# Optimization experiments

Hardware: AMD Instinct MI355X
Metric: run time of the kernel (lower is better)

Reference implementation:

```python
import jax, jax.numpy as jnp
import numpy as np

B, D, H = 4096, 2048, 2048

def setup_inputs() -> dict:
    key = jax.random.key(0)
    ks = jax.random.split(key, 16)
    s = 0.02  # small scale to keep tanh/sigmoid out of saturation
    inp = {
        'input_': jax.random.normal(ks[0], (B, D), jnp.float32),
        'h_prev': jax.random.normal(ks[1], (B, H), jnp.float32),
        'c_prev': jax.random.normal(ks[2], (B, H), jnp.float32),
        'w_xi': jax.random.normal(ks[3], (D, H), jnp.float32) * s,
        'w_hi': jax.random.normal(ks[4], (H, H), jnp.float32) * s,
        'w_ci': jax.random.normal(ks[5], (H, H), jnp.float32) * s,
        'w_xf': jax.random.normal(ks[6], (D, H), jnp.float32) * s,
        'w_hf': jax.random.normal(ks[7], (H, H), jnp.float32) * s,
        'w_cf': jax.random.normal(ks[8], (H, H), jnp.float32) * s,
        'w_xg': jax.random.normal(ks[9], (D, H), jnp.float32) * s,
        'w_hg': jax.random.normal(ks[10], (H, H), jnp.float32) * s,
        'w_xo': jax.random.normal(ks[11], (D, H), jnp.float32) * s,
        'w_ho': jax.random.normal(ks[12], (H, H), jnp.float32) * s,
        'w_co': jax.random.normal(ks[13], (H, H), jnp.float32) * s,
        'w_c':  jax.random.normal(ks[14], (H, H), jnp.float32) * s,
        'w_i':  jax.random.normal(ks[15], (D, H), jnp.float32) * s,
        'b_i': jnp.zeros((H,), jnp.float32),
        'b_f': jnp.zeros((H,), jnp.float32),
        'b_g': jnp.zeros((H,), jnp.float32),
        'b_o': jnp.zeros((H,), jnp.float32),
    }
    return inp

def reference(input_, h_prev, c_prev,
              w_xi, w_hi, w_ci, w_xf, w_hf, w_cf, w_xg, w_hg,
              w_xo, w_ho, w_co, w_c, w_i,
              b_i, b_f, b_g, b_o):
    # Fuse the x- and h-path GEMMs into concatenated matmuls (math-identical).
    wx = jnp.concatenate([w_xi, w_xf, w_xg, w_xo, w_i], axis=1)   # [D, 5H]
    wh = jnp.concatenate([w_hi, w_hf, w_hg, w_ho], axis=1)        # [H, 4H]
    wc = jnp.concatenate([w_ci, w_cf], axis=1)                    # [H, 2H]
    xz = input_ @ wx                                              # [B, 5H]
    hz = h_prev @ wh                                              # [B, 4H]
    cz = c_prev @ wc                                              # [B, 2H]
    Hd = w_hi.shape[0]
    i = xz[:, 0*Hd:1*Hd] + hz[:, 0*Hd:1*Hd] + cz[:, 0*Hd:1*Hd] + b_i
    f = xz[:, 1*Hd:2*Hd] + hz[:, 1*Hd:2*Hd] + cz[:, 1*Hd:2*Hd] + b_f
    g = xz[:, 2*Hd:3*Hd] + hz[:, 2*Hd:3*Hd] + b_g
    c = jax.nn.sigmoid(f) * c_prev + jax.nn.sigmoid(i) * jnp.tanh(g)
    o = xz[:, 3*Hd:4*Hd] + hz[:, 3*Hd:4*Hd] + c @ w_co + b_o
    h = jnp.tanh(o) * (jnp.tanh(c) @ w_c + xz[:, 4*Hd:5*Hd])
    return (h, c)
```

## Files before the change

### kernel.cpp

```cpp
#include <hip/hip_runtime.h>
#include <cstdint>
#include <cstddef>

typedef unsigned short u16;
typedef __bf16 bf16x8 __attribute__((ext_vector_type(8)));
typedef float f32x4 __attribute__((ext_vector_type(4)));
typedef u16 u16x8 __attribute__((ext_vector_type(8)));

#define B_DIM 4096
#define H_DIM 2048
#define BH 8388608

__device__ __forceinline__ float b2f(u16 x) {
  union { uint32_t u; float f; } v;
  v.u = ((uint32_t)x) << 16;
  return v.f;
}
__device__ __forceinline__ u16 f2b(float f) {
  union { float f; uint32_t u; } v;
  v.f = f;
  uint32_t r = v.u + 0x7FFFu + ((v.u >> 16) & 1u);
  return (u16)(r >> 16);
}
__device__ __forceinline__ float sigm(float x) { return 1.0f / (1.0f + __expf(-x)); }

typedef __attribute__((address_space(1))) void gv_t;
typedef __attribute__((address_space(3))) void lv_t;
__device__ __forceinline__ void g2lds16(const void* g, void* l) {
  __builtin_amdgcn_global_load_lds((gv_t*)g, (lv_t*)l, 16, 0, 0);
}

struct CvtParams { const float* src[3]; u16* dst[3]; };

__global__ __launch_bounds__(256) void cvt_k(CvtParams p) {
  const float* __restrict__ s = p.src[blockIdx.y];
  u16* __restrict__ d = p.dst[blockIdx.y];
  size_t idx = ((size_t)blockIdx.x * 256 + threadIdx.x) * 8;
  float4 a = *(const float4*)(s + idx);
  float4 b = *(const float4*)(s + idx + 4);
  u16x8 o;
  o[0] = f2b(a.x); o[1] = f2b(a.y); o[2] = f2b(a.z); o[3] = f2b(a.w);
  o[4] = f2b(b.x); o[5] = f2b(b.y); o[6] = f2b(b.z); o[7] = f2b(b.w);
  *(u16x8*)(d + idx) = o;
}

struct TransParams {
  const float* src[13];
  u16* dst[13];
  int dstride[13];
};

__global__ __launch_bounds__(256) void transpose_k(TransParams p) {
  __shared__ u16 lds[64][72];
  const int mat = blockIdx.z;
  const float* __restrict__ src = p.src[mat];
  u16* __restrict__ dst = p.dst[mat];
  const int dstride = p.dstride[mat];
  const int tk = blockIdx.y * 64;
  const int tn = blockIdx.x * 64;
  const int t = threadIdx.x;
  const int lr = t >> 3;
  const int lc = (t & 7) * 8;
#pragma unroll
  for (int half = 0; half < 2; half++) {
    int r = lr + half * 32;
    const float4* g = (const float4*)(src + (size_t)(tk + r) * 2048 + tn + lc);
    float4 a = g[0], b = g[1];
    u16x8 t8;
    t8[0] = f2b(a.x); t8[1] = f2b(a.y); t8[2] = f2b(a.z); t8[3] = f2b(a.w);
    t8[4] = f2b(b.x); t8[5] = f2b(b.y); t8[6] = f2b(b.z); t8[7] = f2b(b.w);
    *(u16x8*)&lds[r][lc] = t8;
  }
  __syncthreads();
#pragma unroll
  for (int half = 0; half < 2; half++) {
    int n = lr + half * 32;
    u16x8 tmp;
#pragma unroll
    for (int j = 0; j < 8; j++) tmp[j] = lds[lc + j][n];
    *(u16x8*)(dst + (size_t)(tn + n) * dstride + tk + lc) = tmp;
  }
}

struct GemmDesc {
  const u16* A0; const u16* A1; const u16* A2;
  const u16* Wt; u16* C; int nseg; int addin;
};
struct GemmParams { GemmDesc d[5]; };

__global__ __launch_bounds__(256) void gemm_multi(GemmParams p) {
  const GemmDesc d = p.d[blockIdx.z];
  const int nseg = d.nseg;
  const long Ktot = (long)nseg * 2048;

  __shared__ u16 ldsA[128 * 32];
  __shared__ u16 ldsB[128 * 32];

  const int t = threadIdx.x;
  const int wave = t >> 6, lane = t & 63;
  const int m0 = blockIdx.y * 128, n0 = blockIdx.x * 128;

  const int sr = lane >> 2;
  const int sc = (lane & 3) * 8;
  u16* lA0 = &ldsA[wave * 1024];
  u16* lA1 = lA0 + 512;
  u16* lB0 = &ldsB[wave * 1024];
  u16* lB1 = lB0 + 512;
  const size_t rA0 = (size_t)(m0 + wave * 32 + sr);
  const size_t rB0 = (size_t)(n0 + wave * 32 + sr);

  const int fm = lane & 15, fk = (lane >> 4) * 8;
  const int wm = (wave >> 1) * 64, wn = (wave & 1) * 64;

  f32x4 acc[4][4];
#pragma unroll
  for (int i = 0; i < 4; i++)
#pragma unroll
    for (int j = 0; j < 4; j++) acc[i][j] = (f32x4)0.0f;

  for (int seg = 0; seg < nseg; ++seg) {
    const u16* As = (seg == 0) ? d.A0 : ((seg == 1) ? d.A1 : d.A2);
    const u16* pA0 = As + rA0 * 2048 + sc;
    const u16* pA1 = pA0 + 16 * 2048;
    const u16* pB0 = d.Wt + rB0 * Ktot + (size_t)seg * 2048 + sc;
    const u16* pB1 = pB0 + 16 * Ktot;
    for (int kk = 0; kk < 2048; kk += 32) {
      __syncthreads();
      g2lds16(pA0, lA0);
      g2lds16(pA1, lA1);
      g2lds16(pB0, lB0);
      g2lds16(pB1, lB1);
      __syncthreads();
      bf16x8 af[4], bfr[4];
#pragma unroll
      for (int i = 0; i < 4; i++)
        af[i] = *(const bf16x8*)&ldsA[(wm + i * 16 + fm) * 32 + fk];
#pragma unroll
      for (int j = 0; j < 4; j++)
        bfr[j] = *(const bf16x8*)&ldsB[(wn + j * 16 + fm) * 32 + fk];
#pragma unroll
      for (int i = 0; i < 4; i++)
#pragma unroll
        for (int j = 0; j < 4; j++)
          acc[i][j] = __builtin_amdgcn_mfma_f32_16x16x32_bf16(af[i], bfr[j], acc[i][j], 0, 0, 0);
      pA0 += 32; pA1 += 32; pB0 += 32; pB1 += 32;
    }
  }

  const int quad = lane >> 4;
#pragma unroll
  for (int i = 0; i < 4; i++) {
#pragma unroll
    for (int j = 0; j < 4; j++) {
#pragma unroll
      for (int r = 0; r < 4; r++) {
        size_t row = (size_t)(m0 + wm + i * 16 + quad * 4 + r);
        size_t col = (size_t)(n0 + wn + j * 16 + fm);
        size_t cidx = row * 2048 + col;
        float v = acc[i][j][r];
        if (d.addin) v += b2f(d.C[cidx]);
        d.C[cidx] = f2b(v);
      }
    }
  }
}

__global__ __launch_bounds__(256) void ew1_k(
    u16* __restrict__ zi, const u16* __restrict__ zf, u16* __restrict__ zg,
    const float* __restrict__ cprev, const float* __restrict__ bi,
    const float* __restrict__ bff, const float* __restrict__ bg,
    float* __restrict__ c_out) {
  size_t idx = ((size_t)blockIdx.x * 256 + threadIdx.x) * 8;
  int col = (int)(idx & (H_DIM - 1));
  u16x8 vzi = *(const u16x8*)(zi + idx);
  u16x8 vzf = *(const u16x8*)(zf + idx);
  u16x8 vzg = *(const u16x8*)(zg + idx);
  float4 cp0 = *(const float4*)(cprev + idx);
  float4 cp1 = *(const float4*)(cprev + idx + 4);
  float4 bi0 = *(const float4*)(bi + col), bi1 = *(const float4*)(bi + col + 4);
  float4 bf0 = *(const float4*)(bff + col), bf1 = *(const float4*)(bff + col + 4);
  float4 bg0 = *(const float4*)(bg + col), bg1 = *(const float4*)(bg + col + 4);
  float cpv[8] = {cp0.x, cp0.y, cp0.z, cp0.w, cp1.x, cp1.y, cp1.z, cp1.w};
  float biv[8] = {bi0.x, bi0.y, bi0.z, bi0.w, bi1.x, bi1.y, bi1.z, bi1.w};
  float bfv[8] = {bf0.x, bf0.y, bf0.z, bf0.w, bf1.x, bf1.y, bf1.z, bf1.w};
  float bgv[8] = {bg0.x, bg0.y, bg0.z, bg0.w, bg1.x, bg1.y, bg1.z, bg1.w};
  float cv[8], tcv[8];
#pragma unroll
  for (int e = 0; e < 8; e++) {
    float iv = b2f(vzi[e]) + biv[e];
    float fv = b2f(vzf[e]) + bfv[e];
    float gv = b2f(vzg[e]) + bgv[e];
    float c = sigm(fv) * cpv[e] + sigm(iv) * tanhf(gv);
    cv[e] = c;
    tcv[e] = tanhf(c);
  }
  u16x8 cb8, tc8;
#pragma unroll
  for (int e = 0; e < 8; e++) { cb8[e] = f2b(cv[e]); tc8[e] = f2b(tcv[e]); }
  *(u16x8*)(zi + idx) = cb8;
  *(u16x8*)(zg + idx) = tc8;
  float4 c0 = {cv[0], cv[1], cv[2], cv[3]}, c1 = {cv[4], cv[5], cv[6], cv[7]};
  *(float4*)(c_out + idx) = c0;
  *(float4*)(c_out + idx + 4) = c1;
}

__global__ __launch_bounds__(256) void ew2_k(
    const u16* __restrict__ zo, const u16* __restrict__ zr,
    const float* __restrict__ bo, float* __restrict__ h_out) {
  size_t idx = ((size_t)blockIdx.x * 256 + threadIdx.x) * 8;
  int col = (int)(idx & (H_DIM - 1));
  u16x8 vzo = *(const u16x8*)(zo + idx);
  u16x8 vzr = *(const u16x8*)(zr + idx);
  float4 bo0 = *(const float4*)(bo + col), bo1 = *(const float4*)(bo + col + 4);
  float bov[8] = {bo0.x, bo0.y, bo0.z, bo0.w, bo1.x, bo1.y, bo1.z, bo1.w};
  float hv[8];
#pragma unroll
  for (int e = 0; e < 8; e++) {
    float ov = b2f(vzo[e]) + bov[e];
    hv[e] = tanhf(ov) * b2f(vzr[e]);
  }
  float4 h0 = {hv[0], hv[1], hv[2], hv[3]}, h1 = {hv[4], hv[5], hv[6], hv[7]};
  *(float4*)(h_out + idx) = h0;
  *(float4*)(h_out + idx + 4) = h1;
}

extern "C" void kernel_launch(void* const* d_in, const int* in_sizes, int n_in,
                              void* d_out, int out_size, void* d_ws, size_t ws_size,
                              hipStream_t stream) {
  const float* input_ = (const float*)d_in[0];
  const float* h_prev = (const float*)d_in[1];
  const float* c_prev = (const float*)d_in[2];
  const float* w_xi = (const float*)d_in[3];
  const float* w_hi = (const float*)d_in[4];
  const float* w_ci = (const float*)d_in[5];
  const float* w_xf = (const float*)d_in[6];
  const float* w_hf = (const float*)d_in[7];
  const float* w_cf = (const float*)d_in[8];
  const float* w_xg = (const float*)d_in[9];
  const float* w_hg = (const float*)d_in[10];
  const float* w_xo = (const float*)d_in[11];
  const float* w_ho = (const float*)d_in[12];
  const float* w_co = (const float*)d_in[13];
  const float* w_c  = (const float*)d_in[14];
  const float* w_i  = (const float*)d_in[15];
  const float* b_i  = (const float*)d_in[16];
  const float* b_f  = (const float*)d_in[17];
  const float* b_g  = (const float*)d_in[18];
  const float* b_o  = (const float*)d_in[19];

  u16* ws = (u16*)d_ws;
  u16* WtI  = ws;
  u16* WtF  = WtI  + (size_t)2048 * 6144;
  u16* WtG  = WtF  + (size_t)2048 * 6144;
  u16* WtO  = WtG  + (size_t)2048 * 4096;
  u16* WtR  = WtO  + (size_t)2048 * 4096;
  u16* WtCO = WtR  + (size_t)2048 * 2048;
  u16* WtC  = WtCO + (size_t)2048 * 2048;
  u16* zi   = WtC  + (size_t)2048 * 2048;
  u16* zf   = zi + (size_t)BH;
  u16* zg   = zf + (size_t)BH;
  u16* zo   = zg + (size_t)BH;
  u16* zr   = zo + (size_t)BH;

  u16* ob16 = (u16*)d_out;
  u16* xb = ob16;
  u16* hb = ob16 + (size_t)BH;
  u16* cb = ob16 + (size_t)2 * BH;
  float* out_f = (float*)d_out;
  float* h_out = out_f;
  float* c_out = out_f + (size_t)BH;

  CvtParams cp;
  cp.src[0] = input_; cp.src[1] = h_prev; cp.src[2] = c_prev;
  cp.dst[0] = xb; cp.dst[1] = hb; cp.dst[2] = cb;
  cvt_k<<<dim3(BH / 2048, 3), 256, 0, stream>>>(cp);

  TransParams tp;
  const float* srcs[13] = {w_xi, w_hi, w_ci, w_xf, w_hf, w_cf, w_xg, w_hg, w_xo, w_ho, w_i, w_co, w_c};
  u16* dsts[13] = {WtI, WtI + 2048, WtI + 4096, WtF, WtF + 2048, WtF + 4096,
                   WtG, WtG + 2048, WtO, WtO + 2048, WtR, WtCO, WtC};
  int strides[13] = {6144, 6144, 6144, 6144, 6144, 6144, 4096, 4096, 4096, 4096, 2048, 2048, 2048};
  for (int i = 0; i < 13; i++) { tp.src[i] = srcs[i]; tp.dst[i] = dsts[i]; tp.dstride[i] = strides[i]; }
  transpose_k<<<dim3(32, 32, 13), 256, 0, stream>>>(tp);

  GemmParams g1;
  g1.d[0] = {xb, hb, cb, WtI, zi, 3, 0};
  g1.d[1] = {xb, hb, cb, WtF, zf, 3, 0};
  g1.d[2] = {xb, hb, nullptr, WtG, zg, 2, 0};
  g1.d[3] = {xb, hb, nullptr, WtO, zo, 2, 0};
  g1.d[4] = {xb, nullptr, nullptr, WtR, zr, 1, 0};
  gemm_multi<<<dim3(16, 32, 5), 256, 0, stream>>>(g1);

  ew1_k<<<dim3(BH / 2048), 256, 0, stream>>>(zi, zf, zg, c_prev, b_i, b_f, b_g, c_out);

  GemmParams g2;
  g2.d[0] = {zi, nullptr, nullptr, WtCO, zo, 1, 1};
  g2.d[1] = {zg, nullptr, nullptr, WtC, zr, 1, 1};
  g2.d[2] = g2.d[0]; g2.d[3] = g2.d[0]; g2.d[4] = g2.d[0];
  gemm_multi<<<dim3(16, 32, 2), 256, 0, stream>>>(g2);

  ew2_k<<<dim3(BH / 2048), 256, 0, stream>>>(zo, zr, b_o, h_out);
}
```

Before: 929.9 us.

## Deepen GEMM K-tile to 64 with XOR-swizzled LDS and fuse output GEMMs with epilogue

The GEMM main loop moves into a shared helper that loads 64-wide K tiles into LDS with an XOR swizzle, halving the number of barrier pairs per K and avoiding LDS bank conflicts. The second-stage GEMM launch and the ew2 elementwise kernel are replaced by one gemm_res kernel. Each block computes both the c@w_co and tanh(c)@w_c tiles, holding the first result in registers as packed bf16, then applies tanh and the multiply directly to write h. This removes the read-modify-write of zo/zr and one kernel launch. The cost is halved grid parallelism in the fused kernel (512 blocks doing twice the work each), plus more LDS use and register pressure.

```diff
diff --git a/kernel.cpp b/kernel.cpp
--- a/kernel.cpp
+++ b/kernel.cpp
@@ -82,9 +82,63 @@
   }
 }
 
+__device__ __forceinline__ void seg2048(
+    const u16* __restrict__ Aseg,
+    const u16* __restrict__ Wseg,
+    long ldW,
+    u16* ldsA, u16* ldsB,
+    int wave, int lane,
+    int wm, int wn, int fm, int fkc,
+    f32x4 (&acc)[4][4]) {
+  const int sr8 = lane >> 3;
+  const int slot = lane & 7;
+  const int sc = ((slot ^ sr8) << 3);
+  const u16* pA[4]; const u16* pB[4];
+  u16* lA[4]; u16* lB[4];
+#pragma unroll
+  for (int i = 0; i < 4; i++) {
+    int rl = wave * 32 + i * 8;
+    pA[i] = Aseg + (size_t)(rl + sr8) * 2048 + sc;
+    pB[i] = Wseg + (size_t)(rl + sr8) * ldW + sc;
+    lA[i] = ldsA + rl * 64;
+    lB[i] = ldsB + rl * 64;
+  }
+  const int x7 = fm & 7;
+  int raBase[4], rbBase[4];
+#pragma unroll
+  for (int i = 0; i < 4; i++) {
+    raBase[i] = (wm + i * 16 + fm) * 64;
+    rbBase[i] = (wn + i * 16 + fm) * 64;
+  }
+  for (int it = 0; it < 32; ++it) {
+    __syncthreads();
+#pragma unroll
+    for (int i = 0; i < 4; i++) { g2lds16(pA[i], lA[i]); g2lds16(pB[i], lB[i]); }
+    __syncthreads();
+#pragma unroll
+    for (int ks = 0; ks < 2; ks++) {
+      const int c = ks * 4 + fkc;
+      const int so = ((c ^ x7) << 3);
+      bf16x8 af[4], bfr[4];
+#pragma unroll
+      for (int i = 0; i < 4; i++) {
+        af[i] = *(const bf16x8*)&ldsA[raBase[i] + so];
+        bfr[i] = *(const bf16x8*)&ldsB[rbBase[i] + so];
+      }
+#pragma unroll
+      for (int i = 0; i < 4; i++)
+#pragma unroll
+        for (int j = 0; j < 4; j++)
+          acc[i][j] = __builtin_amdgcn_mfma_f32_16x16x32_bf16(af[i], bfr[j], acc[i][j], 0, 0, 0);
+    }
+#pragma unroll
+    for (int i = 0; i < 4; i++) { pA[i] += 64; pB[i] += 64; }
+  }
+}
+
 struct GemmDesc {
   const u16* A0; const u16* A1; const u16* A2;
-  const u16* Wt; u16* C; int nseg; int addin;
+  const u16* Wt; u16* C; int nseg;
 };
 struct GemmParams { GemmDesc d[5]; };
 
@@ -93,23 +147,13 @@
   const int nseg = d.nseg;
   const long Ktot = (long)nseg * 2048;
 
-  __shared__ u16 ldsA[128 * 32];
-  __shared__ u16 ldsB[128 * 32];
+  __shared__ u16 ldsA[128 * 64];
+  __shared__ u16 ldsB[128 * 64];
 
   const int t = threadIdx.x;
   const int wave = t >> 6, lane = t & 63;
   const int m0 = blockIdx.y * 128, n0 = blockIdx.x * 128;
-
-  const int sr = lane >> 2;
-  const int sc = (lane & 3) * 8;
-  u16* lA0 = &ldsA[wave * 1024];
-  u16* lA1 = lA0 + 512;
-  u16* lB0 = &ldsB[wave * 1024];
-  u16* lB1 = lB0 + 512;
-  const size_t rA0 = (size_t)(m0 + wave * 32 + sr);
-  const size_t rB0 = (size_t)(n0 + wave * 32 + sr);
-
-  const int fm = lane & 15, fk = (lane >> 4) * 8;
+  const int fm = lane & 15, fkc = lane >> 4;
   const int wm = (wave >> 1) * 64, wn = (wave & 1) * 64;
 
   f32x4 acc[4][4];
@@ -120,31 +164,9 @@
 
   for (int seg = 0; seg < nseg; ++seg) {
     const u16* As = (seg == 0) ? d.A0 : ((seg == 1) ? d.A1 : d.A2);
-    const u16* pA0 = As + rA0 * 2048 + sc;
-    const u16* pA1 = pA0 + 16 * 2048;
-    const u16* pB0 = d.Wt + rB0 * Ktot + (size_t)seg * 2048 + sc;
-    const u16* pB1 = pB0 + 16 * Ktot;
-    for (int kk = 0; kk < 2048; kk += 32) {
-      __syncthreads();
-      g2lds16(pA0, lA0);
-      g2lds16(pA1, lA1);
-      g2lds16(pB0, lB0);
-      g2lds16(pB1, lB1);
-      __syncthreads();
-      bf16x8 af[4], bfr[4];
-#pragma unroll
-      for (int i = 0; i < 4; i++)
-        af[i] = *(const bf16x8*)&ldsA[(wm + i * 16 + fm) * 32 + fk];
-#pragma unroll
-      for (int j = 0; j < 4; j++)
-        bfr[j] = *(const bf16x8*)&ldsB[(wn + j * 16 + fm) * 32 + fk];
-#pragma unroll
-      for (int i = 0; i < 4; i++)
-#pragma unroll
-        for (int j = 0; j < 4; j++)
-          acc[i][j] = __builtin_amdgcn_mfma_f32_16x16x32_bf16(af[i], bfr[j], acc[i][j], 0, 0, 0);
-      pA0 += 32; pA1 += 32; pB0 += 32; pB1 += 32;
-    }
+    seg2048(As + (size_t)m0 * 2048,
+            d.Wt + (size_t)n0 * Ktot + (size_t)seg * 2048, Ktot,
+            ldsA, ldsB, wave, lane, wm, wn, fm, fkc, acc);
   }
 
   const int quad = lane >> 4;
@@ -156,10 +178,68 @@
       for (int r = 0; r < 4; r++) {
         size_t row = (size_t)(m0 + wm + i * 16 + quad * 4 + r);
         size_t col = (size_t)(n0 + wn + j * 16 + fm);
-        size_t cidx = row * 2048 + col;
-        float v = acc[i][j][r];
-        if (d.addin) v += b2f(d.C[cidx]);
-        d.C[cidx] = f2b(v);
+        d.C[row * 2048 + col] = f2b(acc[i][j][r]);
+      }
+    }
+  }
+}
+
+__global__ __launch_bounds__(256) void gemm_res(
+    const u16* __restrict__ cb16, const u16* __restrict__ tcb16,
+    const u16* __restrict__ WtCO, const u16* __restrict__ WtC,
+    const u16* __restrict__ zo, const u16* __restrict__ zr,
+    const float* __restrict__ bo, float* __restrict__ h_out) {
+  __shared__ u16 ldsA[128 * 64];
+  __shared__ u16 ldsB[128 * 64];
+
+  const int t = threadIdx.x;
+  const int wave = t >> 6, lane = t & 63;
+  const int m0 = blockIdx.y * 128, n0 = blockIdx.x * 128;
+  const int fm = lane & 15, fkc = lane >> 4;
+  const int wm = (wave >> 1) * 64, wn = (wave & 1) * 64;
+
+  f32x4 acc[4][4];
+#pragma unroll
+  for (int i = 0; i < 4; i++)
+#pragma unroll
+    for (int j = 0; j < 4; j++) acc[i][j] = (f32x4)0.0f;
+
+  seg2048(cb16 + (size_t)m0 * 2048, WtCO + (size_t)n0 * 2048, 2048,
+          ldsA, ldsB, wave, lane, wm, wn, fm, fkc, acc);
+
+  uint32_t t1p[4][4][2];
+#pragma unroll
+  for (int i = 0; i < 4; i++)
+#pragma unroll
+    for (int j = 0; j < 4; j++)
+#pragma unroll
+      for (int pp = 0; pp < 2; pp++)
+        t1p[i][j][pp] = (uint32_t)f2b(acc[i][j][2 * pp]) |
+                        ((uint32_t)f2b(acc[i][j][2 * pp + 1]) << 16);
+
+#pragma unroll
+  for (int i = 0; i < 4; i++)
+#pragma unroll
+    for (int j = 0; j < 4; j++) acc[i][j] = (f32x4)0.0f;
+
+  seg2048(tcb16 + (size_t)m0 * 2048, WtC + (size_t)n0 * 2048, 2048,
+          ldsA, ldsB, wave, lane, wm, wn, fm, fkc, acc);
+
+  const int quad = lane >> 4;
+#pragma unroll
+  for (int i = 0; i < 4; i++) {
+#pragma unroll
+    for (int j = 0; j < 4; j++) {
+      int col = n0 + wn + j * 16 + fm;
+      float bov = bo[col];
+#pragma unroll
+      for (int r = 0; r < 4; r++) {
+        size_t row = (size_t)(m0 + wm + i * 16 + quad * 4 + r);
+        size_t idx = row * 2048 + (size_t)col;
+        float t1 = b2f((u16)(t1p[i][j][r >> 1] >> ((r & 1) * 16)));
+        float ov = b2f(zo[idx]) + t1 + bov;
+        float hv = tanhf(ov) * (b2f(zr[idx]) + acc[i][j][r]);
+        h_out[idx] = hv;
       }
     }
   }
@@ -202,26 +282,6 @@
   float4 c0 = {cv[0], cv[1], cv[2], cv[3]}, c1 = {cv[4], cv[5], cv[6], cv[7]};
   *(float4*)(c_out + idx) = c0;
   *(float4*)(c_out + idx + 4) = c1;
-}
-
-__global__ __launch_bounds__(256) void ew2_k(
-    const u16* __restrict__ zo, const u16* __restrict__ zr,
-    const float* __restrict__ bo, float* __restrict__ h_out) {
-  size_t idx = ((size_t)blockIdx.x * 256 + threadIdx.x) * 8;
-  int col = (int)(idx & (H_DIM - 1));
-  u16x8 vzo = *(const u16x8*)(zo + idx);
-  u16x8 vzr = *(const u16x8*)(zr + idx);
-  float4 bo0 = *(const float4*)(bo + col), bo1 = *(const float4*)(bo + col + 4);
-  float bov[8] = {bo0.x, bo0.y, bo0.z, bo0.w, bo1.x, bo1.y, bo1.z, bo1.w};
-  float hv[8];
-#pragma unroll
-  for (int e = 0; e < 8; e++) {
-    float ov = b2f(vzo[e]) + bov[e];
-    hv[e] = tanhf(ov) * b2f(vzr[e]);
-  }
-  float4 h0 = {hv[0], hv[1], hv[2], hv[3]}, h1 = {hv[4], hv[5], hv[6], hv[7]};
-  *(float4*)(h_out + idx) = h0;
-  *(float4*)(h_out + idx + 4) = h1;
 }
 
 extern "C" void kernel_launch(void* const* d_in, const int* in_sizes, int n_in,
@@ -284,20 +344,14 @@
   transpose_k<<<dim3(32, 32, 13), 256, 0, stream>>>(tp);
 
   GemmParams g1;
-  g1.d[0] = {xb, hb, cb, WtI, zi, 3, 0};
-  g1.d[1] = {xb, hb, cb, WtF, zf, 3, 0};
-  g1.d[2] = {xb, hb, nullptr, WtG, zg, 2, 0};
-  g1.d[3] = {xb, hb, nullptr, WtO, zo, 2, 0};
-  g1.d[4] = {xb, nullptr, nullptr, WtR, zr, 1, 0};
+  g1.d[0] = {xb, hb, cb, WtI, zi, 3};
+  g1.d[1] = {xb, hb, cb, WtF, zf, 3};
+  g1.d[2] = {xb, hb, nullptr, WtG, zg, 2};
+  g1.d[3] = {xb, hb, nullptr, WtO, zo, 2};
+  g1.d[4] = {xb, nullptr, nullptr, WtR, zr, 1};
   gemm_multi<<<dim3(16, 32, 5), 256, 0, stream>>>(g1);
 
   ew1_k<<<dim3(BH / 2048), 256, 0, stream>>>(zi, zf, zg, c_prev, b_i, b_f, b_g, c_out);
 
-  GemmParams g2;
-  g2.d[0] = {zi, nullptr, nullptr, WtCO, zo, 1, 1};
-  g2.d[1] = {zg, nullptr, nullptr, WtC, zr, 1, 1};
-  g2.d[2] = g2.d[0]; g2.d[3] = g2.d[0]; g2.d[4] = g2.d[0];
-  gemm_multi<<<dim3(16, 32, 2), 256, 0, stream>>>(g2);
-
-  ew2_k<<<dim3(BH / 2048), 256, 0, stream>>>(zo, zr, b_o, h_out);
-}
+  gemm_res<<<dim3(16, 32), 256, 0, stream>>>(zi, zg, WtCO, WtC, zo, zr, b_o, h_out);
+}
```

Result: faster. 891.7 us (-4.1%).
